# Kernel tuning notes

Measured on AMD Instinct MI355X. Metric: run time of the kernel, lower is better.

Reference implementation:

```python
import jax, jax.numpy as jnp
import numpy as np

NUM_PROTOTYPES = 512
NUM_BLOCKS = 8
D_MODEL = 1024
D_BLOCK = D_MODEL // NUM_BLOCKS


def setup_inputs() -> dict:
    key = jax.random.key(0)
    kq, km = jax.random.split(key)
    queries = jax.random.normal(kq, (8, 1024, D_MODEL), dtype=jnp.float32)
    # learned codebook: nn.Embedding(num_blocks*num_prototypes, d_block), normal init
    mem = jax.random.normal(km, (NUM_BLOCKS * NUM_PROTOTYPES, D_BLOCK), dtype=jnp.float32)
    return {"queries": queries, "mem": mem}


def reference(queries, mem):
    B, N, _ = queries.shape
    m, p, d = NUM_BLOCKS, NUM_PROTOTYPES, D_BLOCK
    q = queries.reshape(B, N, m, d)                 # [B,N,m,d]
    codes = mem.reshape(m, p, d)                    # [m,p,d]
    # Squared distances restricted to each query's own block (the only entries
    # the original consumes via distances[i, :, i]):
    #   ||q||^2 - 2 q.c + ||c||^2
    dots = jnp.einsum('bnmd,mpd->bnmp', q, codes)   # [B,N,m,p]
    qn = jnp.sum(q * q, axis=-1)                    # [B,N,m]
    cn = jnp.sum(codes * codes, axis=-1)            # [m,p]
    dist = qn[..., None] - 2.0 * dots + cn[None, None]
    local = jnp.argmin(dist, axis=-1)               # [B,N,m], first-min tiebreak like torch max of -dist
    indices = local + jnp.arange(m, dtype=local.dtype)[None, None, :] * p
    emb = codes[jnp.arange(m)[None, None, :], local]          # [B,N,m,d]
    emb = emb.reshape(B, N, m * d)
    # straight-through estimator
    emb_st = jax.lax.stop_gradient(emb - queries) + queries
    vq_loss = jnp.asarray(0.0, dtype=queries.dtype)
    commitment_loss = jnp.mean((jax.lax.stop_gradient(emb) - queries) ** 2)
    return emb_st, indices, vq_loss, commitment_loss
```

## Files before the change

kernel.cpp:

```cpp
#include <hip/hip_runtime.h>

#define NPROTO 512
#define NBLK 8
#define DB 128
#define DM 1024
#define TMR 128
#define PC 128

#define IDX_OFF  8388608
#define VQ_OFF   8454144
#define CL_OFF   8454145

typedef unsigned short u16;
typedef __attribute__((ext_vector_type(8))) _Float16 f16x8;
typedef __attribute__((ext_vector_type(4))) float f32x4;

#define BH_B   0u
#define BL_B   1048576u
#define CN_B   2097152u
#define PART_B 2113536u
#define WS_NEED (PART_B + 4096u)

__device__ __forceinline__ void gl_lds16(const u16* g, u16* l) {
    __builtin_amdgcn_global_load_lds(
        (const __attribute__((address_space(1))) unsigned int*)g,
        (__attribute__((address_space(3))) unsigned int*)l, 16, 0, 0);
}

__global__ __launch_bounds__(256) void vq_prep(const float* __restrict__ src,
                                               u16* __restrict__ hi,
                                               u16* __restrict__ lo,
                                               float* __restrict__ cn) {
    const int t  = threadIdx.x;
    const int p  = blockIdx.x * 32 + (t >> 3);
    const int e0 = (t & 7) * 16;
    const float* s = src + (size_t)p * DB + e0;
    float sq = 0.f;
    #pragma unroll
    for (int j = 0; j < 4; ++j) {
        float4 v = *(const float4*)(s + j * 4);
        ushort4 h, l;
        float x; _Float16 hf;
        #define S1(c, f) x = v.c; hf = (_Float16)x; h.f = __builtin_bit_cast(u16, hf); \
            hf = (_Float16)(x - (float)hf); l.f = __builtin_bit_cast(u16, hf); sq += x * x;
        S1(x, x) S1(y, y) S1(z, z) S1(w, w)
        #undef S1
        size_t o4 = ((size_t)p * DB + e0) / 4 + j;
        ((ushort4*)hi)[o4] = h;
        ((ushort4*)lo)[o4] = l;
    }
    sq += __shfl_xor(sq, 1, 64);
    sq += __shfl_xor(sq, 2, 64);
    sq += __shfl_xor(sq, 4, 64);
    if ((t & 7) == 0) cn[p] = sq;
}

__global__ __launch_bounds__(512, 2) void vq_fused(
        const float* __restrict__ q, const float* __restrict__ mem,
        const u16* __restrict__ bh, const u16* __restrict__ bl,
        const float* __restrict__ cn, float* __restrict__ out,
        float* __restrict__ partials) {
    __shared__ u16 Bt[2][2][PC][64];
    __shared__ float qn_lds[TMR];
    __shared__ int   bp[TMR];
    __shared__ float red[32];

    const int t    = threadIdx.x;
    const int lane = t & 63;
    const int w    = t >> 6;
    const int lrow = lane & 15;
    const int lk   = lane >> 4;
    const int m    = blockIdx.y;
    const int bn0  = blockIdx.x * TMR;

    const u16* plbase = (w & 1) ? bl : bh;
    const int  p_l    = (w >> 1) * 32 + (lane >> 3);
    const int  sl     = lane & 7;
    const u16* g0 = plbase + ((size_t)(m * NPROTO + p_l)) * DB
                           + ((sl ^ (p_l & 7)) * 8);

#define STAGE(st_, nb_) do { \
    const u16* gs_ = g0 + ((st_) >> 1) * (PC * DB) + ((st_) & 1) * 64; \
    u16* lb_ = &Bt[(nb_)][w & 1][(w >> 1) * 32][0]; \
    gl_lds16(gs_,           lb_); \
    gl_lds16(gs_ + 8 * DB,  lb_ + 8 * 64); \
    gl_lds16(gs_ + 16 * DB, lb_ + 16 * 64); \
    gl_lds16(gs_ + 24 * DB, lb_ + 24 * 64); \
} while (0)

    STAGE(0, 0);

    f16x8 ah[4], al[4];
    float qnp = 0.f;
    #pragma unroll
    for (int kst = 0; kst < 4; ++kst) {
        const float* src = q + (size_t)(bn0 + w * 16 + lrow) * DM
                             + m * DB + kst * 32 + lk * 8;
        float4 v0 = *(const float4*)src;
        float4 v1 = *(const float4*)(src + 4);
        f16x8 hv, lv;
        float x; _Float16 hh;
        #define SA(e, val) x = (val); hh = (_Float16)x; hv[e] = hh; \
            lv[e] = (_Float16)(x - (float)hh); qnp += x * x;
        SA(0, v0.x) SA(1, v0.y) SA(2, v0.z) SA(3, v0.w)
        SA(4, v1.x) SA(5, v1.y) SA(6, v1.z) SA(7, v1.w)
        #undef SA
        ah[kst] = hv; al[kst] = lv;
    }
    qnp += __shfl_xor(qnp, 16, 64);
    qnp += __shfl_xor(qnp, 32, 64);
    if (lk == 0) qn_lds[w * 16 + lrow] = qnp;

    float bestv[4]; int besti[4];
    #pragma unroll
    for (int r = 0; r < 4; ++r) { bestv[r] = 3.4e38f; besti[r] = 0; }

    f32x4 acc[8];
    #pragma unroll
    for (int fj = 0; fj < 8; ++fj) acc[fj] = (f32x4){0.f, 0.f, 0.f, 0.f};

    const float* cnbase = cn + m * NPROTO + lrow;

    __syncthreads();

    float qnr[4];
    #pragma unroll
    for (int r = 0; r < 4; ++r) qnr[r] = qn_lds[w * 16 + lk * 4 + r];

    #pragma unroll
    for (int st = 0; st < 8; ++st) {
        const int s = st & 1, buf = st & 1, ch = st >> 1;
        if (st < 7) STAGE(st + 1, buf ^ 1);
        #pragma unroll
        for (int kk = 0; kk < 2; ++kk) {
            const int kst = s * 2 + kk;
            #pragma unroll
            for (int fj = 0; fj < 8; ++fj) {
                const int rowb = fj * 16 + lrow;
                const int so   = (((kk * 4 + lk) ^ (rowb & 7)) * 8);
                f16x8 Bh = *(const f16x8*)&Bt[buf][0][rowb][so];
                f16x8 Bl = *(const f16x8*)&Bt[buf][1][rowb][so];
                f32x4 a = acc[fj];
                a = __builtin_amdgcn_mfma_f32_16x16x32_f16(ah[kst], Bh, a, 0, 0, 0);
                a = __builtin_amdgcn_mfma_f32_16x16x32_f16(al[kst], Bh, a, 0, 0, 0);
                a = __builtin_amdgcn_mfma_f32_16x16x32_f16(ah[kst], Bl, a, 0, 0, 0);
                acc[fj] = a;
            }
        }
        if (s == 1) {
            #pragma unroll
            for (int fj = 0; fj < 8; ++fj) {
                const int   ploc = ch * PC + fj * 16 + lrow;
                const float cnv  = cnbase[ch * PC + fj * 16];
                #pragma unroll
                for (int r = 0; r < 4; ++r) {
                    float d = (qnr[r] - 2.0f * acc[fj][r]) + cnv;
                    if (d < bestv[r]) { bestv[r] = d; besti[r] = ploc; }
                }
                acc[fj] = (f32x4){0.f, 0.f, 0.f, 0.f};
            }
        }
        __syncthreads();
    }

    #pragma unroll
    for (int r = 0; r < 4; ++r) {
        float v = bestv[r]; int ix = besti[r];
        #pragma unroll
        for (int off = 1; off < 16; off <<= 1) {
            float v2 = __shfl_xor(v, off, 64);
            int  ix2 = __shfl_xor(ix, off, 64);
            if (v2 < v || (v2 == v && ix2 < ix)) { v = v2; ix = ix2; }
        }
        bestv[r] = v; besti[r] = ix;
    }

    if (lrow == 0) {
        float lp = 0.f;
        #pragma unroll
        for (int r = 0; r < 4; ++r) {
            int row = w * 16 + lk * 4 + r;
            bp[row] = besti[r];
            out[(size_t)IDX_OFF + (size_t)(bn0 + row) * NBLK + m] =
                (float)(m * NPROTO + besti[r]);
            lp += bestv[r];
        }
        red[w * 4 + lk] = lp;
    }
    __syncthreads();

    {
        int row = t >> 2, qt = t & 3;
        int bpi = bp[row];
        const float* cv = mem + ((size_t)(m * NPROTO + bpi)) * DB + qt * 32;
        float* ov = out + (size_t)(bn0 + row) * DM + m * DB + qt * 32;
        #pragma unroll
        for (int j = 0; j < 8; ++j)
            *(float4*)(ov + j * 4) = *(const float4*)(cv + j * 4);
    }
    if (t == 0) {
        float s = 0.f;
        #pragma unroll
        for (int i = 0; i < 32; ++i) s += red[i];
        partials[blockIdx.y * gridDim.x + blockIdx.x] = s;
    }
#undef STAGE
}

__global__ __launch_bounds__(256) void vq_init(const float* __restrict__ mem,
                                               float* __restrict__ cn) {
    int p = blockIdx.x * 256 + threadIdx.x;
    const float* c = mem + (size_t)p * DB;
    float s = 0.f;
    #pragma unroll 8
    for (int k = 0; k < DB; k += 4) {
        float4 v = *(const float4*)(c + k);
        s += v.x * v.x + v.y * v.y + v.z * v.z + v.w * v.w;
    }
    cn[p] = s;
}

__global__ __launch_bounds__(256, 1) void vq_main_f32(const float* __restrict__ q,
                                                      const float* __restrict__ mem,
                                                      const float* __restrict__ cn,
                                                      float* __restrict__ out,
                                                      float* __restrict__ partials) {
    __shared__ float q_lds[128 * 132];
    __shared__ float c_lds[128 * 132];
    __shared__ float red[256];

    const int t    = threadIdx.x;
    const int tile = blockIdx.x;
    const int m    = blockIdx.y;
    const int tr   = t >> 4;
    const int tc   = t & 15;
    const int bn0  = tile * 128;

    const float* qbase = q + (size_t)bn0 * DM + m * DB;
    #pragma unroll
    for (int it = 0; it < 16; ++it) {
        int idx = it * 256 + t;
        int row = idx >> 5;
        int c4  = (idx & 31) << 2;
        *(float4*)&q_lds[row * 132 + c4] = *(const float4*)(qbase + (size_t)row * DM + c4);
    }

    float bestv[8]; int besti[8];
    #pragma unroll
    for (int i = 0; i < 8; ++i) { bestv[i] = 3.4e38f; besti[i] = 0; }
    const float* cbase = mem + (size_t)m * NPROTO * DB;

    for (int ch = 0; ch < 4; ++ch) {
        __syncthreads();
        const float* cb = cbase + (size_t)ch * PC * DB;
        #pragma unroll
        for (int it = 0; it < 16; ++it) {
            int idx = it * 256 + t;
            int row = idx >> 5;
            int c4  = (idx & 31) << 2;
            *(float4*)&c_lds[row * 132 + c4] = *(const float4*)(cb + row * DB + c4);
        }
        __syncthreads();

        float acc[8][8];
        #pragma unroll
        for (int i = 0; i < 8; ++i)
            #pragma unroll
            for (int j = 0; j < 8; ++j) acc[i][j] = 0.f;

        for (int d4 = 0; d4 < DB; d4 += 4) {
            float4 qa[8], cvv[8];
            #pragma unroll
            for (int i = 0; i < 8; ++i) qa[i] = *(const float4*)&q_lds[(tr + 16 * i) * 132 + d4];
            #pragma unroll
            for (int j = 0; j < 8; ++j) cvv[j] = *(const float4*)&c_lds[(tc + 16 * j) * 132 + d4];
            #pragma unroll
            for (int i = 0; i < 8; ++i)
                #pragma unroll
                for (int j = 0; j < 8; ++j) {
                    acc[i][j] += qa[i].x * cvv[j].x; acc[i][j] += qa[i].y * cvv[j].y;
                    acc[i][j] += qa[i].z * cvv[j].z; acc[i][j] += qa[i].w * cvv[j].w;
                }
        }
        #pragma unroll
        for (int i = 0; i < 8; ++i)
            #pragma unroll
            for (int j = 0; j < 8; ++j) {
                int lp = ch * PC + tc + 16 * j;
                float dist = cn[m * NPROTO + lp] - 2.0f * acc[i][j];
                if (dist < bestv[i]) { bestv[i] = dist; besti[i] = lp; }
            }
    }

    #pragma unroll
    for (int i = 0; i < 8; ++i) {
        float v = bestv[i]; int ix = besti[i];
        #pragma unroll
        for (int off = 1; off < 16; off <<= 1) {
            float v2 = __shfl_xor(v, off, 64);
            int  ix2 = __shfl_xor(ix, off, 64);
            if (v2 < v || (v2 == v && ix2 < ix)) { v = v2; ix = ix2; }
        }
        bestv[i] = v; besti[i] = ix;
    }

    float lacc = 0.f;
    #pragma unroll
    for (int i = 0; i < 8; ++i) {
        int row = tr + 16 * i;
        int bn  = bn0 + row;
        const float* cvec = cbase + (size_t)besti[i] * DB;
        float* orow = out + (size_t)bn * DM + m * DB;
        #pragma unroll
        for (int h = 0; h < 2; ++h) {
            int col = h * 64 + tc * 4;
            float4 c4v = *(const float4*)(cvec + col);
            *(float4*)(orow + col) = c4v;
            float4 qv2 = *(const float4*)&q_lds[row * 132 + col];
            float dx = c4v.x - qv2.x, dy = c4v.y - qv2.y;
            float dz = c4v.z - qv2.z, dw = c4v.w - qv2.w;
            lacc += dx * dx + dy * dy + dz * dz + dw * dw;
        }
        if (tc == 0)
            out[(size_t)IDX_OFF + (size_t)bn * NBLK + m] = (float)(m * NPROTO + besti[i]);
    }

    red[t] = lacc;
    __syncthreads();
    for (int s = 128; s > 0; s >>= 1) {
        if (t < s) red[t] += red[t + s];
        __syncthreads();
    }
    if (t == 0) partials[blockIdx.y * gridDim.x + blockIdx.x] = red[0];
}

__global__ __launch_bounds__(256) void vq_final(const float* __restrict__ partials,
                                                float* __restrict__ out, int n) {
    __shared__ float red[256];
    int t = threadIdx.x;
    float v = (t < n) ? partials[t] : 0.f;
    if (t + 256 < n) v += partials[t + 256];
    red[t] = v;
    __syncthreads();
    for (int s = 128; s > 0; s >>= 1) {
        if (t < s) red[t] += red[t + s];
        __syncthreads();
    }
    if (t == 0) {
        out[VQ_OFF] = 0.f;
        out[CL_OFF] = red[0] / 8388608.0f;
    }
}

extern "C" void kernel_launch(void* const* d_in, const int* in_sizes, int n_in,
                              void* d_out, int out_size, void* d_ws, size_t ws_size,
                              hipStream_t stream) {
    const float* q   = (const float*)d_in[0];
    const float* mem = (const float*)d_in[1];
    float* out = (float*)d_out;
    char* ws = (char*)d_ws;

    if (ws_size >= (size_t)WS_NEED) {
        u16*   bhp = (u16*)(ws + BH_B);
        u16*   blp = (u16*)(ws + BL_B);
        float* cnp = (float*)(ws + CN_B);
        float* partials = (float*)(ws + PART_B);

        vq_prep<<<128, 256, 0, stream>>>(mem, bhp, blp, cnp);
        dim3 grid(64, 8);
        vq_fused<<<grid, 512, 0, stream>>>(q, mem, bhp, blp, cnp, out, partials);
        vq_final<<<1, 256, 0, stream>>>(partials, out, 512);
    } else {
        float* cn = (float*)ws;
        float* partials = cn + 4096;
        vq_init<<<16, 256, 0, stream>>>(mem, cn);
        dim3 grid(64, 8);
        vq_main_f32<<<grid, 256, 0, stream>>>(q, mem, cn, out, partials);
        vq_final<<<1, 256, 0, stream>>>(partials, out, 512);
    }
}
```

Before: 61.56 us.

## Restructure fused VQ kernel to 32-row tiles with 32x32 MFMA and direct B loads

Tiles change from 128 query rows per block to 32 rows, so the grid grows from 512 to 2048 blocks. The query tile is split into fp16 hi/lo parts and kept in LDS. Each wave takes 128 prototypes and reads the codebook operands straight from global memory into registers, feeding 32x32x16 MFMAs instead of double-buffered global-to-LDS staging with 16x16 MFMAs. The argmin is reduced across waves through LDS, and the final partial-sum reduction now handles more partials. The aim is more parallelism and less LDS staging and synchronisation, at the cost of reloading the codebook from global/L2 far more often.

```diff
diff --git a/kernel.cpp b/kernel.cpp
--- a/kernel.cpp
+++ b/kernel.cpp
@@ -4,8 +4,6 @@
 #define NBLK 8
 #define DB 128
 #define DM 1024
-#define TMR 128
-#define PC 128
 
 #define IDX_OFF  8388608
 #define VQ_OFF   8454144
@@ -13,19 +11,13 @@
 
 typedef unsigned short u16;
 typedef __attribute__((ext_vector_type(8))) _Float16 f16x8;
-typedef __attribute__((ext_vector_type(4))) float f32x4;
+typedef __attribute__((ext_vector_type(16))) float f32x16;
 
 #define BH_B   0u
 #define BL_B   1048576u
 #define CN_B   2097152u
 #define PART_B 2113536u
-#define WS_NEED (PART_B + 4096u)
-
-__device__ __forceinline__ void gl_lds16(const u16* g, u16* l) {
-    __builtin_amdgcn_global_load_lds(
-        (const __attribute__((address_space(1))) unsigned int*)g,
-        (__attribute__((address_space(3))) unsigned int*)l, 16, 0, 0);
-}
+#define WS_NEED (PART_B + 8192u)
 
 __global__ __launch_bounds__(256) void vq_prep(const float* __restrict__ src,
                                                u16* __restrict__ hi,
@@ -55,156 +47,154 @@
     if ((t & 7) == 0) cn[p] = sq;
 }
 
-__global__ __launch_bounds__(512, 2) void vq_fused(
+__device__ __forceinline__ unsigned cvt2(float x, float y, unsigned& lo) {
+    _Float16 hx = (_Float16)x, hy = (_Float16)y;
+    _Float16 lx = (_Float16)(x - (float)hx), ly = (_Float16)(y - (float)hy);
+    lo = (unsigned)__builtin_bit_cast(u16, lx) | ((unsigned)__builtin_bit_cast(u16, ly) << 16);
+    return (unsigned)__builtin_bit_cast(u16, hx) | ((unsigned)__builtin_bit_cast(u16, hy) << 16);
+}
+
+__global__ __launch_bounds__(256, 2) void vq_fused(
         const float* __restrict__ q, const float* __restrict__ mem,
         const u16* __restrict__ bh, const u16* __restrict__ bl,
         const float* __restrict__ cn, float* __restrict__ out,
         float* __restrict__ partials) {
-    __shared__ u16 Bt[2][2][PC][64];
-    __shared__ float qn_lds[TMR];
-    __shared__ int   bp[TMR];
-    __shared__ float red[32];
+    __shared__ __align__(16) char smem0[16896];
+    __shared__ u16  sidxv[4][32][33];
+    __shared__ float finalv[4][32];
+    __shared__ int   finali[4][32];
+    __shared__ float qn_lds[32];
+    __shared__ int   bp[32];
+    __shared__ float lossbuf[32];
+
+    u16   (*Ap)[8][32][16] = (u16 (*)[8][32][16])smem0;
+    float (*sval)[32][33]  = (float (*)[32][33])smem0;
 
     const int t    = threadIdx.x;
     const int lane = t & 63;
     const int w    = t >> 6;
-    const int lrow = lane & 15;
-    const int lk   = lane >> 4;
+    const int col  = lane & 31;
+    const int kg   = lane >> 5;
     const int m    = blockIdx.y;
-    const int bn0  = blockIdx.x * TMR;
-
-    const u16* plbase = (w & 1) ? bl : bh;
-    const int  p_l    = (w >> 1) * 32 + (lane >> 3);
-    const int  sl     = lane & 7;
-    const u16* g0 = plbase + ((size_t)(m * NPROTO + p_l)) * DB
-                           + ((sl ^ (p_l & 7)) * 8);
-
-#define STAGE(st_, nb_) do { \
-    const u16* gs_ = g0 + ((st_) >> 1) * (PC * DB) + ((st_) & 1) * 64; \
-    u16* lb_ = &Bt[(nb_)][w & 1][(w >> 1) * 32][0]; \
-    gl_lds16(gs_,           lb_); \
-    gl_lds16(gs_ + 8 * DB,  lb_ + 8 * 64); \
-    gl_lds16(gs_ + 16 * DB, lb_ + 16 * 64); \
-    gl_lds16(gs_ + 24 * DB, lb_ + 24 * 64); \
-} while (0)
-
-    STAGE(0, 0);
-
-    f16x8 ah[4], al[4];
-    float qnp = 0.f;
-    #pragma unroll
-    for (int kst = 0; kst < 4; ++kst) {
-        const float* src = q + (size_t)(bn0 + w * 16 + lrow) * DM
-                             + m * DB + kst * 32 + lk * 8;
-        float4 v0 = *(const float4*)src;
-        float4 v1 = *(const float4*)(src + 4);
-        f16x8 hv, lv;
-        float x; _Float16 hh;
-        #define SA(e, val) x = (val); hh = (_Float16)x; hv[e] = hh; \
-            lv[e] = (_Float16)(x - (float)hh); qnp += x * x;
-        SA(0, v0.x) SA(1, v0.y) SA(2, v0.z) SA(3, v0.w)
-        SA(4, v1.x) SA(5, v1.y) SA(6, v1.z) SA(7, v1.w)
-        #undef SA
-        ah[kst] = hv; al[kst] = lv;
-    }
-    qnp += __shfl_xor(qnp, 16, 64);
-    qnp += __shfl_xor(qnp, 32, 64);
-    if (lk == 0) qn_lds[w * 16 + lrow] = qnp;
-
-    float bestv[4]; int besti[4];
-    #pragma unroll
-    for (int r = 0; r < 4; ++r) { bestv[r] = 3.4e38f; besti[r] = 0; }
-
-    f32x4 acc[8];
-    #pragma unroll
-    for (int fj = 0; fj < 8; ++fj) acc[fj] = (f32x4){0.f, 0.f, 0.f, 0.f};
-
-    const float* cnbase = cn + m * NPROTO + lrow;
-
-    __syncthreads();
-
-    float qnr[4];
-    #pragma unroll
-    for (int r = 0; r < 4; ++r) qnr[r] = qn_lds[w * 16 + lk * 4 + r];
-
-    #pragma unroll
-    for (int st = 0; st < 8; ++st) {
-        const int s = st & 1, buf = st & 1, ch = st >> 1;
-        if (st < 7) STAGE(st + 1, buf ^ 1);
-        #pragma unroll
-        for (int kk = 0; kk < 2; ++kk) {
-            const int kst = s * 2 + kk;
-            #pragma unroll
-            for (int fj = 0; fj < 8; ++fj) {
-                const int rowb = fj * 16 + lrow;
-                const int so   = (((kk * 4 + lk) ^ (rowb & 7)) * 8);
-                f16x8 Bh = *(const f16x8*)&Bt[buf][0][rowb][so];
-                f16x8 Bl = *(const f16x8*)&Bt[buf][1][rowb][so];
-                f32x4 a = acc[fj];
-                a = __builtin_amdgcn_mfma_f32_16x16x32_f16(ah[kst], Bh, a, 0, 0, 0);
-                a = __builtin_amdgcn_mfma_f32_16x16x32_f16(al[kst], Bh, a, 0, 0, 0);
-                a = __builtin_amdgcn_mfma_f32_16x16x32_f16(ah[kst], Bl, a, 0, 0, 0);
-                acc[fj] = a;
-            }
-        }
-        if (s == 1) {
-            #pragma unroll
-            for (int fj = 0; fj < 8; ++fj) {
-                const int   ploc = ch * PC + fj * 16 + lrow;
-                const float cnv  = cnbase[ch * PC + fj * 16];
-                #pragma unroll
-                for (int r = 0; r < 4; ++r) {
-                    float d = (qnr[r] - 2.0f * acc[fj][r]) + cnv;
-                    if (d < bestv[r]) { bestv[r] = d; besti[r] = ploc; }
-                }
-                acc[fj] = (f32x4){0.f, 0.f, 0.f, 0.f};
-            }
-        }
-        __syncthreads();
-    }
-
-    #pragma unroll
-    for (int r = 0; r < 4; ++r) {
-        float v = bestv[r]; int ix = besti[r];
-        #pragma unroll
-        for (int off = 1; off < 16; off <<= 1) {
-            float v2 = __shfl_xor(v, off, 64);
-            int  ix2 = __shfl_xor(ix, off, 64);
-            if (v2 < v || (v2 == v && ix2 < ix)) { v = v2; ix = ix2; }
-        }
-        bestv[r] = v; besti[r] = ix;
-    }
-
-    if (lrow == 0) {
-        float lp = 0.f;
-        #pragma unroll
-        for (int r = 0; r < 4; ++r) {
-            int row = w * 16 + lk * 4 + r;
-            bp[row] = besti[r];
-            out[(size_t)IDX_OFF + (size_t)(bn0 + row) * NBLK + m] =
-                (float)(m * NPROTO + besti[r]);
-            lp += bestv[r];
-        }
-        red[w * 4 + lk] = lp;
-    }
-    __syncthreads();
+    const int bn0  = blockIdx.x * 32;
 
     {
-        int row = t >> 2, qt = t & 3;
-        int bpi = bp[row];
-        const float* cv = mem + ((size_t)(m * NPROTO + bpi)) * DB + qt * 32;
-        float* ov = out + (size_t)(bn0 + row) * DM + m * DB + qt * 32;
-        #pragma unroll
-        for (int j = 0; j < 8; ++j)
-            *(float4*)(ov + j * 4) = *(const float4*)(cv + j * 4);
+        const int row = t >> 3, g = t & 7;
+        const float* src = q + (size_t)(bn0 + row) * DM + m * DB + g * 16;
+        float4 v0 = ((const float4*)src)[0];
+        float4 v1 = ((const float4*)src)[1];
+        float4 v2 = ((const float4*)src)[2];
+        float4 v3 = ((const float4*)src)[3];
+        float sq = v0.x*v0.x+v0.y*v0.y+v0.z*v0.z+v0.w*v0.w
+                 + v1.x*v1.x+v1.y*v1.y+v1.z*v1.z+v1.w*v1.w
+                 + v2.x*v2.x+v2.y*v2.y+v2.z*v2.z+v2.w*v2.w
+                 + v3.x*v3.x+v3.y*v3.y+v3.z*v3.z+v3.w*v3.w;
+        unsigned l0,l1,l2,l3,l4,l5,l6,l7;
+        unsigned h0 = cvt2(v0.x, v0.y, l0), h1 = cvt2(v0.z, v0.w, l1);
+        unsigned h2 = cvt2(v1.x, v1.y, l2), h3 = cvt2(v1.z, v1.w, l3);
+        unsigned h4 = cvt2(v2.x, v2.y, l4), h5 = cvt2(v2.z, v2.w, l5);
+        unsigned h6 = cvt2(v3.x, v3.y, l6), h7 = cvt2(v3.z, v3.w, l7);
+        const int hsw = (row >> 2) & 1;
+        *(uint4*)&Ap[0][g][row][(0 ^ hsw) * 8] = make_uint4(h0, h1, h2, h3);
+        *(uint4*)&Ap[0][g][row][(1 ^ hsw) * 8] = make_uint4(h4, h5, h6, h7);
+        *(uint4*)&Ap[1][g][row][(0 ^ hsw) * 8] = make_uint4(l0, l1, l2, l3);
+        *(uint4*)&Ap[1][g][row][(1 ^ hsw) * 8] = make_uint4(l4, l5, l6, l7);
+        sq += __shfl_xor(sq, 1, 64);
+        sq += __shfl_xor(sq, 2, 64);
+        sq += __shfl_xor(sq, 4, 64);
+        if (g == 0) qn_lds[row] = sq;
+    }
+    __syncthreads();
+
+    const int pbase = w * 128;
+    const u16* bh_l = bh + (size_t)(m * NPROTO + pbase + col) * DB + kg * 8;
+    const u16* bl_l = bl + (size_t)(m * NPROTO + pbase + col) * DB + kg * 8;
+    const int ahalf = (kg ^ ((col >> 2) & 1)) * 8;
+
+    float bestv[16]; int besti[16];
+    #pragma unroll
+    for (int r = 0; r < 16; ++r) { bestv[r] = 3.4e38f; besti[r] = 0; }
+
+    #pragma unroll 1
+    for (int c = 0; c < 4; ++c) {
+        const float cnv = cn[m * NPROTO + pbase + c * 32 + col];
+        const u16* bhc = bh_l + (size_t)c * 32 * DB;
+        const u16* blc = bl_l + (size_t)c * 32 * DB;
+        f32x16 aA, aB;
+        #pragma unroll
+        for (int r = 0; r < 16; ++r) { aA[r] = 0.f; aB[r] = 0.f; }
+        #pragma unroll
+        for (int kst = 0; kst < 8; ++kst) {
+            f16x8 Bh = *(const f16x8*)(bhc + kst * 16);
+            f16x8 Bl = *(const f16x8*)(blc + kst * 16);
+            f16x8 Ah = *(const f16x8*)&Ap[0][kst][col][ahalf];
+            f16x8 Al = *(const f16x8*)&Ap[1][kst][col][ahalf];
+            aA = __builtin_amdgcn_mfma_f32_32x32x16_f16(Ah, Bh, aA, 0, 0, 0);
+            aB = __builtin_amdgcn_mfma_f32_32x32x16_f16(Al, Bh, aB, 0, 0, 0);
+            aB = __builtin_amdgcn_mfma_f32_32x32x16_f16(Ah, Bl, aB, 0, 0, 0);
+        }
+        const int ix = pbase + c * 32 + col;
+        #pragma unroll
+        for (int r = 0; r < 16; ++r) {
+            float d = cnv - 2.0f * (aA[r] + aB[r]);
+            if (d < bestv[r]) { bestv[r] = d; besti[r] = ix; }
+        }
+    }
+    __syncthreads();
+
+    #pragma unroll
+    for (int r = 0; r < 16; ++r) {
+        int row = (r & 3) + 8 * (r >> 2) + 4 * kg;
+        sval[w][row][col]  = bestv[r];
+        sidxv[w][row][col] = (u16)besti[r];
+    }
+    __syncthreads();
+
+    {
+        const int rrow = col, seg = kg;
+        float bv = 3.4e38f; int bi = 0x7fffffff;
+        #pragma unroll
+        for (int c2 = 0; c2 < 16; ++c2) {
+            float v = sval[w][rrow][seg * 16 + c2];
+            int  ix = sidxv[w][rrow][seg * 16 + c2];
+            if (v < bv || (v == bv && ix < bi)) { bv = v; bi = ix; }
+        }
+        float v2 = __shfl_xor(bv, 32, 64);
+        int   i2 = __shfl_xor(bi, 32, 64);
+        if (v2 < bv || (v2 == bv && i2 < bi)) { bv = v2; bi = i2; }
+        if (kg == 0) { finalv[w][rrow] = bv; finali[w][rrow] = bi; }
+    }
+    __syncthreads();
+
+    if (t < 32) {
+        float bv = finalv[0][t]; int bi = finali[0][t];
+        #pragma unroll
+        for (int w2 = 1; w2 < 4; ++w2) {
+            float v2 = finalv[w2][t]; int i2 = finali[w2][t];
+            if (v2 < bv || (v2 == bv && i2 < bi)) { bv = v2; bi = i2; }
+        }
+        bp[t] = bi;
+        out[(size_t)IDX_OFF + (size_t)(bn0 + t) * NBLK + m] =
+            (float)(m * NPROTO + bi);
+        lossbuf[t] = bv + qn_lds[t];
+    }
+    __syncthreads();
+
+    {
+        const int row = t >> 3, g = t & 7;
+        const float* cv = mem + ((size_t)(m * NPROTO + bp[row])) * DB + g * 16;
+        float* ov = out + (size_t)(bn0 + row) * DM + m * DB + g * 16;
+        ((float4*)ov)[0] = ((const float4*)cv)[0];
+        ((float4*)ov)[1] = ((const float4*)cv)[1];
+        ((float4*)ov)[2] = ((const float4*)cv)[2];
+        ((float4*)ov)[3] = ((const float4*)cv)[3];
     }
     if (t == 0) {
         float s = 0.f;
         #pragma unroll
-        for (int i = 0; i < 32; ++i) s += red[i];
+        for (int i = 0; i < 32; ++i) s += lossbuf[i];
         partials[blockIdx.y * gridDim.x + blockIdx.x] = s;
     }
-#undef STAGE
 }
 
 __global__ __launch_bounds__(256) void vq_init(const float* __restrict__ mem,
@@ -252,7 +242,7 @@
 
     for (int ch = 0; ch < 4; ++ch) {
         __syncthreads();
-        const float* cb = cbase + (size_t)ch * PC * DB;
+        const float* cb = cbase + (size_t)ch * 128 * DB;
         #pragma unroll
         for (int it = 0; it < 16; ++it) {
             int idx = it * 256 + t;
@@ -286,7 +276,7 @@
         for (int i = 0; i < 8; ++i)
             #pragma unroll
             for (int j = 0; j < 8; ++j) {
-                int lp = ch * PC + tc + 16 * j;
+                int lp = ch * 128 + tc + 16 * j;
                 float dist = cn[m * NPROTO + lp] - 2.0f * acc[i][j];
                 if (dist < bestv[i]) { bestv[i] = dist; besti[i] = lp; }
             }
@@ -313,10 +303,10 @@
         float* orow = out + (size_t)bn * DM + m * DB;
         #pragma unroll
         for (int h = 0; h < 2; ++h) {
-            int col = h * 64 + tc * 4;
-            float4 c4v = *(const float4*)(cvec + col);
-            *(float4*)(orow + col) = c4v;
-            float4 qv2 = *(const float4*)&q_lds[row * 132 + col];
+            int colx = h * 64 + tc * 4;
+            float4 c4v = *(const float4*)(cvec + colx);
+            *(float4*)(orow + colx) = c4v;
+            float4 qv2 = *(const float4*)&q_lds[row * 132 + colx];
             float dx = c4v.x - qv2.x, dy = c4v.y - qv2.y;
             float dz = c4v.z - qv2.z, dw = c4v.w - qv2.w;
             lacc += dx * dx + dy * dy + dz * dz + dw * dw;
@@ -338,8 +328,8 @@
                                                 float* __restrict__ out, int n) {
     __shared__ float red[256];
     int t = threadIdx.x;
-    float v = (t < n) ? partials[t] : 0.f;
-    if (t + 256 < n) v += partials[t + 256];
+    float v = 0.f;
+    for (int i = t; i < n; i += 256) v += partials[i];
     red[t] = v;
     __syncthreads();
     for (int s = 128; s > 0; s >>= 1) {
@@ -367,9 +357,9 @@
         float* partials = (float*)(ws + PART_B);
 
         vq_prep<<<128, 256, 0, stream>>>(mem, bhp, blp, cnp);
-        dim3 grid(64, 8);
-        vq_fused<<<grid, 512, 0, stream>>>(q, mem, bhp, blp, cnp, out, partials);
-        vq_final<<<1, 256, 0, stream>>>(partials, out, 512);
+        dim3 grid(256, 8);
+        vq_fused<<<grid, 256, 0, stream>>>(q, mem, bhp, blp, cnp, out, partials);
+        vq_final<<<1, 256, 0, stream>>>(partials, out, 2048);
     } else {
         float* cn = (float*)ws;
         float* partials = cn + 4096;
```

New measurement: 100.5 us. 63.3% more time.
